# Performance work log

Hardware: AMD Instinct MI355X
Metric: run time of the kernel (lower is better)

## Reference

```python
import jax, jax.numpy as jnp
import numpy as np

B, C_IN, H, W = 4, 512, 188, 188
SHARED_CH = 64
NUM_CLASS = 3
M = 200
NUM_MAX = 500
STRIDE = 8
PCR = (-75.2, -75.2, -2.0, 75.2, 75.2, 4.0)
VOX = (0.1, 0.1, 0.15)
OUT_CH = (2, 1, 3, 2, 1, 3)  # center, center_z, dim, rot, iou, hm
MIN_RADIUS = 2.0
OVERLAP = 0.1
INIT_BIAS = -2.19


def conv3x3(x, w):
    return jax.lax.conv_general_dilated(x, w, (1, 1), 'SAME',
                                        dimension_numbers=('NCHW', 'OIHW', 'NCHW'))


def bn_relu(x, p):
    # p: [4, C] = gamma, beta, running_mean, running_var (inference-mode BN)
    g, b, m, v = p[0], p[1], p[2], p[3]
    scale = (g * jax.lax.rsqrt(v + 1e-5))[None, :, None, None]
    y = (x - m[None, :, None, None]) * scale + b[None, :, None, None]
    return jax.nn.relu(y)


def gaussian_radius(height, width, min_overlap):
    # Faithful to OpenPCDet centernet_utils.gaussian_radius
    b1 = height + width
    c1 = width * height * (1 - min_overlap) / (1 + min_overlap)
    sq1 = jnp.sqrt(jnp.maximum(b1 * b1 - 4.0 * c1, 0.0))
    r1 = (b1 + sq1) / 2.0
    b2 = 2.0 * (height + width)
    c2 = (1 - min_overlap) * width * height
    sq2 = jnp.sqrt(jnp.maximum(b2 * b2 - 16.0 * c2, 0.0))
    r2 = (b2 + sq2) / 2.0
    a3 = 4.0 * min_overlap
    b3 = -2.0 * min_overlap * (height + width)
    c3 = (min_overlap - 1.0) * width * height
    sq3 = jnp.sqrt(jnp.maximum(b3 * b3 - 4.0 * a3 * c3, 0.0))
    r3 = (b3 + sq3) / 2.0
    return jnp.minimum(jnp.minimum(r1, r2), r3)


def assign_targets(gt_boxes):
    # gt_boxes: [B, M, 8] = x, y, z, dx, dy, dz, heading, class(1..NUM_CLASS)
    x, y, z = gt_boxes[..., 0], gt_boxes[..., 1], gt_boxes[..., 2]
    dx, dy, dz = gt_boxes[..., 3], gt_boxes[..., 4], gt_boxes[..., 5]
    heading = gt_boxes[..., 6]
    cls = jax.lax.stop_gradient(gt_boxes[..., 7]).astype(jnp.int32)

    cx = jnp.clip((x - PCR[0]) / VOX[0] / STRIDE, 0.0, W - 0.5)  # [B,M]
    cy = jnp.clip((y - PCR[1]) / VOX[1] / STRIDE, 0.0, H - 0.5)
    cxi = jax.lax.stop_gradient(jnp.floor(cx)).astype(jnp.int32)  # .int() trunc == floor (>=0)
    cyi = jax.lax.stop_gradient(jnp.floor(cy)).astype(jnp.int32)

    dxp = dx / VOX[0] / STRIDE
    dyp = dy / VOX[1] / STRIDE
    r = gaussian_radius(dxp, dyp, OVERLAP)
    r = jnp.maximum(jnp.floor(jax.lax.stop_gradient(r)), MIN_RADIUS)  # clamp_min(r.int(), 2)
    sigma = (2.0 * r + 1.0) / 6.0
    valid = (dx > 0) & (dy > 0)  # [B,M]

    ox = jnp.arange(W, dtype=jnp.int32)[None, None, :] - cxi[..., None]  # [B,M,W]
    oy = jnp.arange(H, dtype=jnp.int32)[None, None, :] - cyi[..., None]  # [B,M,H]
    d2 = (oy.astype(jnp.float32) ** 2)[:, :, :, None] + (ox.astype(jnp.float32) ** 2)[:, :, None, :]
    g = jnp.exp(-d2 / (2.0 * sigma * sigma)[:, :, None, None])  # [B,M,H,W]
    win = (jnp.abs(oy)[:, :, :, None] <= r[:, :, None, None]) & \
          (jnp.abs(ox)[:, :, None, :] <= r[:, :, None, None])
    g = jnp.where(win & valid[:, :, None, None], g, 0.0)

    # per-class max-splat (draw_gaussian_to_heatmap uses torch.max overlap)
    heatmap = jnp.stack(
        [jnp.max(jnp.where((cls == c + 1)[:, :, None, None], g, 0.0), axis=1)
         for c in range(NUM_CLASS)], axis=1)  # [B,NUM_CLASS,H,W]

    vf = valid.astype(gt_boxes.dtype)
    vals = jnp.stack([cx - cxi.astype(cx.dtype), cy - cyi.astype(cy.dtype), z,
                      jnp.log(dx), jnp.log(dy), jnp.log(dz),
                      jnp.cos(heading), jnp.sin(heading)], axis=-1) * vf[..., None]
    target_boxes = jnp.zeros((B, NUM_MAX, 8), gt_boxes.dtype).at[:, :M].set(vals)
    ind_vals = (cyi * W + cxi) * valid.astype(jnp.int32)
    inds = jnp.zeros((B, NUM_MAX), jnp.int32).at[:, :M].set(ind_vals)
    mask = jnp.zeros((B, NUM_MAX), jnp.int32).at[:, :M].set(valid.astype(jnp.int32))
    return heatmap, target_boxes, inds, mask


def setup_inputs() -> dict:
    key = jax.random.key(0)
    ks = jax.random.split(key, 16)
    spatial_features = jax.random.normal(ks[0], (B, C_IN, H, W), jnp.float32)
    x = jax.random.uniform(ks[1], (B, M), minval=-70.0, maxval=70.0)
    y = jax.random.uniform(ks[2], (B, M), minval=-70.0, maxval=70.0)
    z = jax.random.uniform(ks[3], (B, M), minval=-1.0, maxval=1.0)
    dx = jax.random.uniform(ks[4], (B, M), minval=1.5, maxval=5.0)
    dy = jax.random.uniform(ks[5], (B, M), minval=1.5, maxval=5.0)
    dz = jax.random.uniform(ks[6], (B, M), minval=1.0, maxval=3.0)
    hd = jax.random.uniform(ks[7], (B, M), minval=-np.pi, maxval=np.pi)
    cls = jax.random.randint(ks[8], (B, M), 1, NUM_CLASS + 1).astype(jnp.float32)
    gt_boxes = jnp.stack([x, y, z, dx, dy, dz, hd, cls], axis=-1)

    def mk_bn(k, lead):
        kk = jax.random.split(k, 4)
        g = 1.0 + 0.1 * jax.random.normal(kk[0], lead + (SHARED_CH,))
        b = 0.1 * jax.random.normal(kk[1], lead + (SHARED_CH,))
        m = 0.1 * jax.random.normal(kk[2], lead + (SHARED_CH,))
        v = jax.random.uniform(kk[3], lead + (SHARED_CH,), minval=0.5, maxval=1.5)
        return jnp.stack([g, b, m, v], axis=len(lead))

    w_shared = jax.random.normal(ks[9], (SHARED_CH, C_IN, 3, 3)) * (1.0 / np.sqrt(C_IN * 9))
    bn_shared = mk_bn(ks[10], ())
    w1_heads = jax.random.normal(ks[11], (6, SHARED_CH, SHARED_CH, 3, 3)) * (1.0 / np.sqrt(SHARED_CH * 9))
    bn_heads = mk_bn(ks[12], (6,))
    w2_heads = jax.random.normal(ks[13], (6, 3, SHARED_CH, 3, 3)) * (1.0 / np.sqrt(SHARED_CH * 9))
    b2_heads = jnp.zeros((6, 3), jnp.float32).at[5].set(INIT_BIAS)  # hm branch bias = -2.19
    return {'spatial_features': spatial_features, 'gt_boxes': gt_boxes,
            'w_shared': w_shared, 'bn_shared': bn_shared,
            'w1_heads': w1_heads, 'bn_heads': bn_heads,
            'w2_heads': w2_heads, 'b2_heads': b2_heads}


def reference(spatial_features, gt_boxes, w_shared, bn_shared,
              w1_heads, bn_heads, w2_heads, b2_heads):
    shared = bn_relu(conv3x3(spatial_features, w_shared), bn_shared)  # [B,64,H,W]

    def branch(w1, bnp, w2, b2):
        h = bn_relu(conv3x3(shared, w1), bnp)
        return conv3x3(h, w2) + b2[None, :, None, None]  # [B,3,H,W] (out padded to 3)

    outs = jax.vmap(branch)(w1_heads, bn_heads, w2_heads, b2_heads)  # [6,B,3,H,W]
    head_out = jnp.concatenate([outs[i, :, :OUT_CH[i]] for i in range(6)], axis=1)  # [B,12,H,W]

    heatmap, target_boxes, inds, mask = assign_targets(gt_boxes)
    return head_out, heatmap, target_boxes, inds, mask
```

## Files before the change

kernel.cpp:

```cpp
#include <hip/hip_runtime.h>
#include <hip/hip_bf16.h>

#define HWD 188
#define NPX (HWD*HWD)
#define NB 4
#define CIN 512
#define CH 64
#define MBOX 200
#define NMAX 500

#define HEAD_SZ (NB*12*NPX)
#define HM_OFF  HEAD_SZ
#define TB_OFF  (HM_OFF + NB*3*NPX)
#define IND_OFF (TB_OFF + NB*NMAX*8)
#define MSK_OFF (IND_OFF + NB*NMAX)

typedef short sh8 __attribute__((ext_vector_type(8)));
typedef float f4 __attribute__((ext_vector_type(4)));
typedef unsigned short us4 __attribute__((ext_vector_type(4)));

__device__ __constant__ int d_cum[6]  = {0, 2, 3, 6, 8, 9};
__device__ __constant__ int d_outc[6] = {2, 1, 3, 2, 1, 3};

__device__ __forceinline__ unsigned short bf16_bits(float v) {
  union { __hip_bfloat16 h; unsigned short u; } cv;
  cv.h = __float2bfloat16(v);
  return cv.u;
}

__global__ __launch_bounds__(256) void wprep(
    const float* __restrict__ ws_, const float* __restrict__ w1_,
    const float* __restrict__ w2_, unsigned short* __restrict__ w1b,
    unsigned short* __restrict__ w2b, unsigned short* __restrict__ w3b) {
  int e = blockIdx.x * 256 + threadIdx.x;
  const int N1 = 9 * 64 * 512;
  const int N2 = 6 * 9 * 64 * 64;
  const int N3 = 6 * 9 * 16 * 64;
  if (e < N1) {
    int tap = e / (64 * 512); int r = e % (64 * 512);
    int oc = r / 512; int ic = r % 512;
    w1b[e] = bf16_bits(ws_[(oc * 512 + ic) * 9 + tap]);
  } else if (e < N1 + N2) {
    int f = e - N1;
    int h = f / (9 * 64 * 64); int r = f % (9 * 64 * 64);
    int tap = r / (64 * 64); int r2 = r % (64 * 64);
    int oc = r2 / 64; int ic = r2 % 64;
    w2b[f] = bf16_bits(w1_[((h * 64 + oc) * 64 + ic) * 9 + tap]);
  } else if (e < N1 + N2 + N3) {
    int f = e - N1 - N2;
    int h = f / (9 * 16 * 64); int r = f % (9 * 16 * 64);
    int tap = r / (16 * 64); int r2 = r % (16 * 64);
    int oc = r2 / 64; int ic = r2 % 64;
    float v = (oc < 3) ? w2_[((h * 3 + oc) * 64 + ic) * 9 + tap] : 0.f;
    w3b[f] = bf16_bits(v);
  }
}

__global__ __launch_bounds__(256) void conv1_mfma(
    const float* __restrict__ sf,
    const unsigned short* __restrict__ wb,
    const float* __restrict__ bnp,
    unsigned short* __restrict__ outp) {
  __shared__ __align__(16) short s_in[10 * 34 * 32];
  const int t = threadIdx.x;
  const int b = blockIdx.y;
  const int rt = blockIdx.x / 6, ct = blockIdx.x % 6;
  const int y0 = rt * 8, x0 = ct * 32;
  const int w = t >> 6, lane = t & 63, ln = lane & 15, kg = lane >> 4;

  f4 acc[4][4];
#pragma unroll
  for (int i = 0; i < 4; ++i)
#pragma unroll
    for (int j = 0; j < 4; ++j) acc[i][j] = (f4){0.f, 0.f, 0.f, 0.f};

  for (int ic0 = 0; ic0 < CIN; ic0 += 32) {
    __syncthreads();
    for (int idx = t; idx < 2720; idx += 256) {
      int c = idx % 34; int rem = idx / 34;
      int r = rem % 10; int iq = rem / 10;
      int gy = y0 - 1 + r, gx = x0 - 1 + c;
      float v0 = 0.f, v1 = 0.f, v2 = 0.f, v3 = 0.f;
      if (gy >= 0 && gy < HWD && gx >= 0 && gx < HWD) {
        const float* p = sf + ((b * CIN + ic0 + iq * 4) * HWD + gy) * HWD + gx;
        v0 = p[0]; v1 = p[NPX]; v2 = p[2 * NPX]; v3 = p[3 * NPX];
      }
      us4 pk = {bf16_bits(v0), bf16_bits(v1), bf16_bits(v2), bf16_bits(v3)};
      *reinterpret_cast<us4*>(&s_in[(r * 34 + c) * 32 + iq * 4]) = pk;
    }
    __syncthreads();
    for (int tap = 0; tap < 9; ++tap) {
      const int ky = tap / 3, kx = tap % 3;
      sh8 af[4];
#pragma unroll
      for (int ot = 0; ot < 4; ++ot)
        af[ot] = *reinterpret_cast<const sh8*>(
            wb + (tap * 64 + ot * 16 + ln) * CIN + ic0 + kg * 8);
#pragma unroll
      for (int nt = 0; nt < 4; ++nt) {
        const int rr = 2 * w + (nt >> 1) + ky;
        const int cc = (nt & 1) * 16 + ln + kx;
        sh8 bf = *reinterpret_cast<const sh8*>(&s_in[(rr * 34 + cc) * 32 + kg * 8]);
#pragma unroll
        for (int ot = 0; ot < 4; ++ot)
          acc[ot][nt] = __builtin_amdgcn_mfma_f32_16x16x32_bf16(
              af[ot], bf, acc[ot][nt], 0, 0, 0);
      }
    }
  }
#pragma unroll
  for (int ot = 0; ot < 4; ++ot) {
    const int ocb = ot * 16 + kg * 4;
    f4 g4 = *reinterpret_cast<const f4*>(bnp + ocb);
    f4 b4 = *reinterpret_cast<const f4*>(bnp + 64 + ocb);
    f4 m4 = *reinterpret_cast<const f4*>(bnp + 128 + ocb);
    f4 v4 = *reinterpret_cast<const f4*>(bnp + 192 + ocb);
    f4 sc, bi;
#pragma unroll
    for (int j = 0; j < 4; ++j) {
      sc[j] = g4[j] * rsqrtf(v4[j] + 1e-5f);
      bi[j] = b4[j] - m4[j] * sc[j];
    }
#pragma unroll
    for (int nt = 0; nt < 4; ++nt) {
      int y = y0 + 2 * w + (nt >> 1);
      int x = x0 + (nt & 1) * 16 + ln;
      if (y < HWD && x < HWD) {
        us4 pk;
#pragma unroll
        for (int j = 0; j < 4; ++j)
          pk[j] = bf16_bits(fmaxf(acc[ot][nt][j] * sc[j] + bi[j], 0.f));
        *reinterpret_cast<us4*>(outp + ((b * HWD + y) * HWD + x) * 64 + ocb) = pk;
      }
    }
  }
}

template<int OCT, int EPI>
__global__ __launch_bounds__(256) void conv_head_mfma(
    const unsigned short* __restrict__ inp,
    const unsigned short* __restrict__ wb0,
    const float* __restrict__ bn0,
    const float* __restrict__ b2,
    unsigned short* __restrict__ outp0,
    float* __restrict__ hout,
    int h_base, long long stride) {
  __shared__ __align__(16) short s_in[10 * 34 * 32];
  const int t = threadIdx.x;
  const int b = blockIdx.y;
  const int h = h_base + blockIdx.z;
  const int rt = blockIdx.x / 6, ct = blockIdx.x % 6;
  const int y0 = rt * 8, x0 = ct * 32;
  const int w = t >> 6, lane = t & 63, ln = lane & 15, kg = lane >> 4;

  const unsigned short* wb = wb0 + h * (9 * OCT * 16 * 64);
  const unsigned short* in_t = (EPI == 1) ? inp + h * stride : inp;

  f4 acc[OCT][4];
#pragma unroll
  for (int i = 0; i < OCT; ++i)
#pragma unroll
    for (int j = 0; j < 4; ++j) acc[i][j] = (f4){0.f, 0.f, 0.f, 0.f};

  for (int ic0 = 0; ic0 < CH; ic0 += 32) {
    __syncthreads();
    for (int idx = t; idx < 1360; idx += 256) {
      int icg = idx & 3; int pix = idx >> 2;
      int c = pix % 34; int r = pix / 34;
      int gy = y0 - 1 + r, gx = x0 - 1 + c;
      sh8 v = (sh8){0, 0, 0, 0, 0, 0, 0, 0};
      if (gy >= 0 && gy < HWD && gx >= 0 && gx < HWD)
        v = *reinterpret_cast<const sh8*>(
            &in_t[((b * HWD + gy) * HWD + gx) * 64 + ic0 + icg * 8]);
      *reinterpret_cast<sh8*>(&s_in[(r * 34 + c) * 32 + icg * 8]) = v;
    }
    __syncthreads();
    for (int tap = 0; tap < 9; ++tap) {
      const int ky = tap / 3, kx = tap % 3;
      sh8 af[OCT];
#pragma unroll
      for (int ot = 0; ot < OCT; ++ot)
        af[ot] = *reinterpret_cast<const sh8*>(
            wb + (tap * OCT * 16 + ot * 16 + ln) * 64 + ic0 + kg * 8);
#pragma unroll
      for (int nt = 0; nt < 4; ++nt) {
        const int rr = 2 * w + (nt >> 1) + ky;
        const int cc = (nt & 1) * 16 + ln + kx;
        sh8 bf = *reinterpret_cast<const sh8*>(&s_in[(rr * 34 + cc) * 32 + kg * 8]);
#pragma unroll
        for (int ot = 0; ot < OCT; ++ot)
          acc[ot][nt] = __builtin_amdgcn_mfma_f32_16x16x32_bf16(
              af[ot], bf, acc[ot][nt], 0, 0, 0);
      }
    }
  }
  if (EPI == 0) {
    unsigned short* outp = outp0 + h * stride;
#pragma unroll
    for (int ot = 0; ot < OCT; ++ot) {
      const int ocb = ot * 16 + kg * 4;
      const float* bnp = bn0 + h * 256;
      f4 g4 = *reinterpret_cast<const f4*>(bnp + ocb);
      f4 b4 = *reinterpret_cast<const f4*>(bnp + 64 + ocb);
      f4 m4 = *reinterpret_cast<const f4*>(bnp + 128 + ocb);
      f4 v4 = *reinterpret_cast<const f4*>(bnp + 192 + ocb);
      f4 sc, bi;
#pragma unroll
      for (int j = 0; j < 4; ++j) {
        sc[j] = g4[j] * rsqrtf(v4[j] + 1e-5f);
        bi[j] = b4[j] - m4[j] * sc[j];
      }
#pragma unroll
      for (int nt = 0; nt < 4; ++nt) {
        int y = y0 + 2 * w + (nt >> 1);
        int x = x0 + (nt & 1) * 16 + ln;
        if (y < HWD && x < HWD) {
          us4 pk;
#pragma unroll
          for (int j = 0; j < 4; ++j)
            pk[j] = bf16_bits(fmaxf(acc[ot][nt][j] * sc[j] + bi[j], 0.f));
          *reinterpret_cast<us4*>(outp + ((b * HWD + y) * HWD + x) * 64 + ocb) = pk;
        }
      }
    }
  } else {
    const int c_off = d_cum[h], noc = d_outc[h];
    const float* bias = b2 + h * 3;
#pragma unroll
    for (int nt = 0; nt < 4; ++nt) {
      int y = y0 + 2 * w + (nt >> 1);
      int x = x0 + (nt & 1) * 16 + ln;
      if (y < HWD && x < HWD) {
#pragma unroll
        for (int j = 0; j < 4; ++j) {
          int oc = kg * 4 + j;
          if (oc < noc)
            hout[(b * 12 + c_off + oc) * NPX + y * HWD + x] =
                acc[0][nt][j] + bias[oc];
        }
      }
    }
  }
}

__global__ __launch_bounds__(256) void targets_kernel(
    const float* __restrict__ gt, float* __restrict__ out, float* __restrict__ boxp) {
  int idx = blockIdx.x * 256 + threadIdx.x;
  if (idx >= NB * NMAX) return;
  int b = idx / NMAX, j = idx - b * NMAX;
  float vals[8] = {0, 0, 0, 0, 0, 0, 0, 0};
  float indf = 0.f, mkf = 0.f;
  if (j < MBOX) {
    const float* g = gt + (b * MBOX + j) * 8;
    float x = g[0], y = g[1], z = g[2], dx = g[3], dy = g[4], dz = g[5];
    float hd = g[6], cls = g[7];
    float cx = (x - (-75.2f)) / 0.1f / 8.0f;
    cx = fminf(fmaxf(cx, 0.0f), (float)HWD - 0.5f);
    float cy = (y - (-75.2f)) / 0.1f / 8.0f;
    cy = fminf(fmaxf(cy, 0.0f), (float)HWD - 0.5f);
    float cxf = floorf(cx), cyf = floorf(cy);
    int cxi = (int)cxf, cyi = (int)cyf;
    float hh = dx / 0.1f / 8.0f;
    float ww = dy / 0.1f / 8.0f;
    const float ov = 0.1f;
    float b1 = hh + ww;
    float c1 = ww * hh * (1.0f - ov) / (1.0f + ov);
    float sq1 = sqrtf(fmaxf(b1 * b1 - 4.0f * c1, 0.0f));
    float r1 = (b1 + sq1) / 2.0f;
    float b2_ = 2.0f * (hh + ww);
    float c2 = (1.0f - ov) * ww * hh;
    float sq2 = sqrtf(fmaxf(b2_ * b2_ - 16.0f * c2, 0.0f));
    float r2 = (b2_ + sq2) / 2.0f;
    float a3 = 4.0f * ov;
    float b3 = -2.0f * ov * (hh + ww);
    float c3 = (ov - 1.0f) * ww * hh;
    float sq3 = sqrtf(fmaxf(b3 * b3 - 4.0f * a3 * c3, 0.0f));
    float r3 = (b3 + sq3) / 2.0f;
    float r = fminf(fminf(r1, r2), r3);
    r = fmaxf(floorf(r), 2.0f);
    float sigma = (2.0f * r + 1.0f) / 6.0f;
    float inv2s2 = 1.0f / (2.0f * sigma * sigma);
    bool valid = (dx > 0.0f) && (dy > 0.0f);
    float vf = valid ? 1.0f : 0.0f;
    vals[0] = (cx - cxf) * vf;
    vals[1] = (cy - cyf) * vf;
    vals[2] = z * vf;
    vals[3] = logf(dx) * vf;
    vals[4] = logf(dy) * vf;
    vals[5] = logf(dz) * vf;
    vals[6] = cosf(hd) * vf;
    vals[7] = sinf(hd) * vf;
    indf = (float)((cyi * HWD + cxi) * (valid ? 1 : 0));
    mkf = vf;
    float* bp = boxp + (b * MBOX + j) * 8;
    bp[0] = cxf; bp[1] = cyf; bp[2] = r; bp[3] = inv2s2;
    bp[4] = valid ? cls : 0.0f; bp[5] = 0.f; bp[6] = 0.f; bp[7] = 0.f;
  }
  float* tb = out + TB_OFF + (b * NMAX + j) * 8;
#pragma unroll
  for (int k = 0; k < 8; ++k) tb[k] = vals[k];
  out[IND_OFF + b * NMAX + j] = indf;
  out[MSK_OFF + b * NMAX + j] = mkf;
}

__global__ __launch_bounds__(256) void heatmap_kernel(
    const float* __restrict__ boxp, float* __restrict__ out) {
  __shared__ float s_bp[MBOX][5];
  const int t = threadIdx.x, b = blockIdx.y;
  for (int e = t; e < MBOX * 5; e += 256) {
    int j = e / 5, k = e - j * 5;
    s_bp[j][k] = boxp[(b * MBOX + j) * 8 + k];
  }
  __syncthreads();
  int p = blockIdx.x * 256 + t;
  if (p >= NPX) return;
  int y = p / HWD, x = p - y * HWD;
  float a0 = 0.f, a1 = 0.f, a2 = 0.f;
  for (int j = 0; j < MBOX; ++j) {
    int c = (int)s_bp[j][4];
    if (c == 0) continue;
    float ox = (float)x - s_bp[j][0];
    float oy = (float)y - s_bp[j][1];
    float r = s_bp[j][2];
    if (fabsf(ox) <= r && fabsf(oy) <= r) {
      float gg = expf(-(ox * ox + oy * oy) * s_bp[j][3]);
      if (c == 1) a0 = fmaxf(a0, gg);
      else if (c == 2) a1 = fmaxf(a1, gg);
      else a2 = fmaxf(a2, gg);
    }
  }
  int base = HM_OFF + (b * 3 * HWD + y) * HWD + x;
  out[base] = a0;
  out[base + NPX] = a1;
  out[base + 2 * NPX] = a2;
}

extern "C" void kernel_launch(void* const* d_in, const int* in_sizes, int n_in,
                              void* d_out, int out_size, void* d_ws, size_t ws_size,
                              hipStream_t stream) {
  (void)in_sizes; (void)n_in; (void)out_size;
  const float* sf = (const float*)d_in[0];
  const float* gt = (const float*)d_in[1];
  const float* w_shared = (const float*)d_in[2];
  const float* bn_shared = (const float*)d_in[3];
  const float* w1 = (const float*)d_in[4];
  const float* bnH = (const float*)d_in[5];
  const float* w2 = (const float*)d_in[6];
  const float* b2 = (const float*)d_in[7];
  float* out = (float*)d_out;
  char* ws = (char*)d_ws;

  const size_t SH = (size_t)NB * NPX * 64 * 2;
  unsigned short* shared_t = (unsigned short*)ws;
  unsigned short* w1b = (unsigned short*)(ws + SH);
  unsigned short* w2b = (unsigned short*)(ws + SH + 589824);
  unsigned short* w3b = (unsigned short*)(ws + SH + 589824 + 442368);
  float* boxp = (float*)(ws + SH + 589824 + 442368 + 110592);
  unsigned short* tmp0 = (unsigned short*)(ws + SH + 589824 + 442368 + 110592 + 25600);

  const size_t need_wide = SH + 589824 + 442368 + 110592 + 25600 + 6 * SH;
  const bool wide = ws_size >= need_wide;
  const long long tstride = wide ? (long long)(SH / 2) : 0LL;

  wprep<<<2232, 256, 0, stream>>>(w_shared, w1, w2, w1b, w2b, w3b);
  conv1_mfma<<<dim3(144, NB), 256, 0, stream>>>(sf, w1b, bn_shared, shared_t);

  if (wide) {
    conv_head_mfma<4, 0><<<dim3(144, NB, 6), 256, 0, stream>>>(
        shared_t, w2b, bnH, nullptr, tmp0, nullptr, 0, tstride);
    conv_head_mfma<1, 1><<<dim3(144, NB, 6), 256, 0, stream>>>(
        tmp0, w3b, nullptr, b2, nullptr, out, 0, tstride);
  } else {
    for (int h = 0; h < 6; ++h) {
      conv_head_mfma<4, 0><<<dim3(144, NB), 256, 0, stream>>>(
          shared_t, w2b, bnH, nullptr, tmp0, nullptr, h, 0);
      conv_head_mfma<1, 1><<<dim3(144, NB), 256, 0, stream>>>(
          tmp0, w3b, nullptr, b2, nullptr, out, h, 0);
    }
  }

  targets_kernel<<<(NB * NMAX + 255) / 256, 256, 0, stream>>>(gt, out, boxp);
  heatmap_kernel<<<dim3((NPX + 255) / 256, NB), 256, 0, stream>>>(boxp, out);
}
```

Measured before the change: 664.6 us.

## Split-K conv1 over input channels with atomic fp32 accumulation and padded LDS

```diff
diff --git a/kernel.cpp b/kernel.cpp
--- a/kernel.cpp
+++ b/kernel.cpp
@@ -15,6 +15,8 @@
 #define IND_OFF (TB_OFF + NB*NMAX*8)
 #define MSK_OFF (IND_OFF + NB*NMAX)
 
+#define PXS 40
+
 typedef short sh8 __attribute__((ext_vector_type(8)));
 typedef float f4 __attribute__((ext_vector_type(4)));
 typedef unsigned short us4 __attribute__((ext_vector_type(4)));
@@ -33,13 +35,14 @@
     const float* __restrict__ w2_, unsigned short* __restrict__ w1b,
     unsigned short* __restrict__ w2b, unsigned short* __restrict__ w3b) {
   int e = blockIdx.x * 256 + threadIdx.x;
-  const int N1 = 9 * 64 * 512;
+  const int N1 = 9 * 16 * 64 * 32;
   const int N2 = 6 * 9 * 64 * 64;
   const int N3 = 6 * 9 * 16 * 64;
   if (e < N1) {
-    int tap = e / (64 * 512); int r = e % (64 * 512);
-    int oc = r / 512; int ic = r % 512;
-    w1b[e] = bf16_bits(ws_[(oc * 512 + ic) * 9 + tap]);
+    int icr = e & 31; int r1 = e >> 5;
+    int oc = r1 & 63; int r2 = r1 >> 6;
+    int icq = r2 & 15; int tap = r2 >> 4;
+    w1b[e] = bf16_bits(ws_[(oc * 512 + icq * 32 + icr) * 9 + tap]);
   } else if (e < N1 + N2) {
     int f = e - N1;
     int h = f / (9 * 64 * 64); int r = f % (9 * 64 * 64);
@@ -56,14 +59,22 @@
   }
 }
 
+__global__ __launch_bounds__(256) void zeroacc(f4* __restrict__ p, int n4) {
+  int i = blockIdx.x * 256 + threadIdx.x;
+  if (i < n4) p[i] = (f4){0.f, 0.f, 0.f, 0.f};
+}
+
+template<int SPLIT>
 __global__ __launch_bounds__(256) void conv1_mfma(
     const float* __restrict__ sf,
     const unsigned short* __restrict__ wb,
     const float* __restrict__ bnp,
+    float* __restrict__ accf,
     unsigned short* __restrict__ outp) {
-  __shared__ __align__(16) short s_in[10 * 34 * 32];
+  __shared__ __align__(16) short s_in[10 * 34 * PXS];
   const int t = threadIdx.x;
   const int b = blockIdx.y;
+  const int ks = SPLIT ? blockIdx.z : 0;
   const int rt = blockIdx.x / 6, ct = blockIdx.x % 6;
   const int y0 = rt * 8, x0 = ct * 32;
   const int w = t >> 6, lane = t & 63, ln = lane & 15, kg = lane >> 4;
@@ -74,7 +85,10 @@
 #pragma unroll
     for (int j = 0; j < 4; ++j) acc[i][j] = (f4){0.f, 0.f, 0.f, 0.f};
 
-  for (int ic0 = 0; ic0 < CIN; ic0 += 32) {
+  const int NSTEP = SPLIT ? 4 : 16;
+  for (int s = 0; s < NSTEP; ++s) {
+    const int icq = ks * 4 + s;
+    const int ic0 = icq * 32;
     __syncthreads();
     for (int idx = t; idx < 2720; idx += 256) {
       int c = idx % 34; int rem = idx / 34;
@@ -86,7 +100,7 @@
         v0 = p[0]; v1 = p[NPX]; v2 = p[2 * NPX]; v3 = p[3 * NPX];
       }
       us4 pk = {bf16_bits(v0), bf16_bits(v1), bf16_bits(v2), bf16_bits(v3)};
-      *reinterpret_cast<us4*>(&s_in[(r * 34 + c) * 32 + iq * 4]) = pk;
+      *reinterpret_cast<us4*>(&s_in[(r * 34 + c) * PXS + iq * 4]) = pk;
     }
     __syncthreads();
     for (int tap = 0; tap < 9; ++tap) {
@@ -95,12 +109,12 @@
 #pragma unroll
       for (int ot = 0; ot < 4; ++ot)
         af[ot] = *reinterpret_cast<const sh8*>(
-            wb + (tap * 64 + ot * 16 + ln) * CIN + ic0 + kg * 8);
+            wb + (((tap * 16 + icq) * 64) + ot * 16 + ln) * 32 + kg * 8);
 #pragma unroll
       for (int nt = 0; nt < 4; ++nt) {
         const int rr = 2 * w + (nt >> 1) + ky;
         const int cc = (nt & 1) * 16 + ln + kx;
-        sh8 bf = *reinterpret_cast<const sh8*>(&s_in[(rr * 34 + cc) * 32 + kg * 8]);
+        sh8 bf = *reinterpret_cast<const sh8*>(&s_in[(rr * 34 + cc) * PXS + kg * 8]);
 #pragma unroll
         for (int ot = 0; ot < 4; ++ot)
           acc[ot][nt] = __builtin_amdgcn_mfma_f32_16x16x32_bf16(
@@ -108,31 +122,75 @@
       }
     }
   }
-#pragma unroll
-  for (int ot = 0; ot < 4; ++ot) {
-    const int ocb = ot * 16 + kg * 4;
-    f4 g4 = *reinterpret_cast<const f4*>(bnp + ocb);
-    f4 b4 = *reinterpret_cast<const f4*>(bnp + 64 + ocb);
-    f4 m4 = *reinterpret_cast<const f4*>(bnp + 128 + ocb);
-    f4 v4 = *reinterpret_cast<const f4*>(bnp + 192 + ocb);
-    f4 sc, bi;
-#pragma unroll
-    for (int j = 0; j < 4; ++j) {
-      sc[j] = g4[j] * rsqrtf(v4[j] + 1e-5f);
-      bi[j] = b4[j] - m4[j] * sc[j];
-    }
-#pragma unroll
-    for (int nt = 0; nt < 4; ++nt) {
-      int y = y0 + 2 * w + (nt >> 1);
-      int x = x0 + (nt & 1) * 16 + ln;
-      if (y < HWD && x < HWD) {
-        us4 pk;
-#pragma unroll
-        for (int j = 0; j < 4; ++j)
-          pk[j] = bf16_bits(fmaxf(acc[ot][nt][j] * sc[j] + bi[j], 0.f));
-        *reinterpret_cast<us4*>(outp + ((b * HWD + y) * HWD + x) * 64 + ocb) = pk;
-      }
-    }
+  if (SPLIT) {
+#pragma unroll
+    for (int ot = 0; ot < 4; ++ot) {
+#pragma unroll
+      for (int nt = 0; nt < 4; ++nt) {
+        int y = y0 + 2 * w + (nt >> 1);
+        int x = x0 + (nt & 1) * 16 + ln;
+        if (y < HWD && x < HWD) {
+          float* p = accf + ((b * HWD + y) * HWD + x) * 64 + ot * 16 + kg * 4;
+#pragma unroll
+          for (int j = 0; j < 4; ++j) atomicAdd(p + j, acc[ot][nt][j]);
+        }
+      }
+    }
+  } else {
+#pragma unroll
+    for (int ot = 0; ot < 4; ++ot) {
+      const int ocb = ot * 16 + kg * 4;
+      f4 g4 = *reinterpret_cast<const f4*>(bnp + ocb);
+      f4 b4 = *reinterpret_cast<const f4*>(bnp + 64 + ocb);
+      f4 m4 = *reinterpret_cast<const f4*>(bnp + 128 + ocb);
+      f4 v4 = *reinterpret_cast<const f4*>(bnp + 192 + ocb);
+      f4 sc, bi;
+#pragma unroll
+      for (int j = 0; j < 4; ++j) {
+        sc[j] = g4[j] * rsqrtf(v4[j] + 1e-5f);
+        bi[j] = b4[j] - m4[j] * sc[j];
+      }
+#pragma unroll
+      for (int nt = 0; nt < 4; ++nt) {
+        int y = y0 + 2 * w + (nt >> 1);
+        int x = x0 + (nt & 1) * 16 + ln;
+        if (y < HWD && x < HWD) {
+          us4 pk;
+#pragma unroll
+          for (int j = 0; j < 4; ++j)
+            pk[j] = bf16_bits(fmaxf(acc[ot][nt][j] * sc[j] + bi[j], 0.f));
+          *reinterpret_cast<us4*>(outp + ((b * HWD + y) * HWD + x) * 64 + ocb) = pk;
+        }
+      }
+    }
+  }
+}
+
+__global__ __launch_bounds__(256) void bn_pack(
+    const float* __restrict__ accf, const float* __restrict__ bnp,
+    unsigned short* __restrict__ outp) {
+  __shared__ float s_sc[64], s_bi[64];
+  const int t = threadIdx.x;
+  if (t < 64) {
+    float g = bnp[t], be = bnp[64 + t], m = bnp[128 + t], v = bnp[192 + t];
+    float sc = g * rsqrtf(v + 1e-5f);
+    s_sc[t] = sc; s_bi[t] = be - m * sc;
+  }
+  __syncthreads();
+  int idx = blockIdx.x * 256 + t;
+  if (idx >= NB * NPX * 4) return;
+  int px = idx >> 2, q = idx & 3;
+  const float* p = accf + (long long)px * 64 + q * 16;
+  unsigned short* o = outp + (long long)px * 64 + q * 16;
+  const int ocb = q * 16;
+#pragma unroll
+  for (int k = 0; k < 4; ++k) {
+    f4 v4 = *reinterpret_cast<const f4*>(p + k * 4);
+    us4 pk;
+#pragma unroll
+    for (int j = 0; j < 4; ++j)
+      pk[j] = bf16_bits(fmaxf(v4[j] * s_sc[ocb + k * 4 + j] + s_bi[ocb + k * 4 + j], 0.f));
+    *reinterpret_cast<us4*>(o + k * 4) = pk;
   }
 }
 
@@ -145,7 +203,7 @@
     unsigned short* __restrict__ outp0,
     float* __restrict__ hout,
     int h_base, long long stride) {
-  __shared__ __align__(16) short s_in[10 * 34 * 32];
+  __shared__ __align__(16) short s_in[10 * 34 * PXS];
   const int t = threadIdx.x;
   const int b = blockIdx.y;
   const int h = h_base + blockIdx.z;
@@ -172,7 +230,7 @@
       if (gy >= 0 && gy < HWD && gx >= 0 && gx < HWD)
         v = *reinterpret_cast<const sh8*>(
             &in_t[((b * HWD + gy) * HWD + gx) * 64 + ic0 + icg * 8]);
-      *reinterpret_cast<sh8*>(&s_in[(r * 34 + c) * 32 + icg * 8]) = v;
+      *reinterpret_cast<sh8*>(&s_in[(r * 34 + c) * PXS + icg * 8]) = v;
     }
     __syncthreads();
     for (int tap = 0; tap < 9; ++tap) {
@@ -186,7 +244,7 @@
       for (int nt = 0; nt < 4; ++nt) {
         const int rr = 2 * w + (nt >> 1) + ky;
         const int cc = (nt & 1) * 16 + ln + kx;
-        sh8 bf = *reinterpret_cast<const sh8*>(&s_in[(rr * 34 + cc) * 32 + kg * 8]);
+        sh8 bf = *reinterpret_cast<const sh8*>(&s_in[(rr * 34 + cc) * PXS + kg * 8]);
 #pragma unroll
         for (int ot = 0; ot < OCT; ++ot)
           acc[ot][nt] = __builtin_amdgcn_mfma_f32_16x16x32_bf16(
@@ -356,14 +414,28 @@
   unsigned short* w2b = (unsigned short*)(ws + SH + 589824);
   unsigned short* w3b = (unsigned short*)(ws + SH + 589824 + 442368);
   float* boxp = (float*)(ws + SH + 589824 + 442368 + 110592);
-  unsigned short* tmp0 = (unsigned short*)(ws + SH + 589824 + 442368 + 110592 + 25600);
-
-  const size_t need_wide = SH + 589824 + 442368 + 110592 + 25600 + 6 * SH;
-  const bool wide = ws_size >= need_wide;
+  const size_t off_acc = SH + 589824 + 442368 + 110592 + 25600;
+  float* accf = (float*)(ws + off_acc);
+  unsigned short* tmp0 = (unsigned short*)(ws + off_acc);
+
+  const size_t ACC_B = (size_t)NB * NPX * 64 * 4;
+  const bool split = ws_size >= off_acc + ACC_B;
+  const bool wide = ws_size >= off_acc + 6 * SH;
   const long long tstride = wide ? (long long)(SH / 2) : 0LL;
 
   wprep<<<2232, 256, 0, stream>>>(w_shared, w1, w2, w1b, w2b, w3b);
-  conv1_mfma<<<dim3(144, NB), 256, 0, stream>>>(sf, w1b, bn_shared, shared_t);
+
+  if (split) {
+    const int n4 = NB * NPX * 16;
+    zeroacc<<<(n4 + 255) / 256, 256, 0, stream>>>((f4*)accf, n4);
+    conv1_mfma<1><<<dim3(144, NB, 4), 256, 0, stream>>>(
+        sf, w1b, nullptr, accf, nullptr);
+    bn_pack<<<(NB * NPX * 4 + 255) / 256, 256, 0, stream>>>(
+        accf, bn_shared, shared_t);
+  } else {
+    conv1_mfma<0><<<dim3(144, NB), 256, 0, stream>>>(
+        sf, w1b, bn_shared, nullptr, shared_t);
+  }
 
   if (wide) {
     conv_head_mfma<4, 0><<<dim3(144, NB, 6), 256, 0, stream>>>(
```

After: 834.8 us. 25.6% more time.

## Double-buffer conv1 input staging with vectorized loads, 512 threads, padded LDS

Applied to the files above, without the earlier changes.

```diff
diff --git a/kernel.cpp b/kernel.cpp
--- a/kernel.cpp
+++ b/kernel.cpp
@@ -15,6 +15,8 @@
 #define IND_OFF (TB_OFF + NB*NMAX*8)
 #define MSK_OFF (IND_OFF + NB*NMAX)
 
+#define PXS 40
+
 typedef short sh8 __attribute__((ext_vector_type(8)));
 typedef float f4 __attribute__((ext_vector_type(4)));
 typedef unsigned short us4 __attribute__((ext_vector_type(4)));
@@ -33,13 +35,14 @@
     const float* __restrict__ w2_, unsigned short* __restrict__ w1b,
     unsigned short* __restrict__ w2b, unsigned short* __restrict__ w3b) {
   int e = blockIdx.x * 256 + threadIdx.x;
-  const int N1 = 9 * 64 * 512;
+  const int N1 = 9 * 16 * 64 * 32;
   const int N2 = 6 * 9 * 64 * 64;
   const int N3 = 6 * 9 * 16 * 64;
   if (e < N1) {
-    int tap = e / (64 * 512); int r = e % (64 * 512);
-    int oc = r / 512; int ic = r % 512;
-    w1b[e] = bf16_bits(ws_[(oc * 512 + ic) * 9 + tap]);
+    int icr = e & 31; int r1 = e >> 5;
+    int oc = r1 & 63; int r2 = r1 >> 6;
+    int icq = r2 & 15; int tap = r2 >> 4;
+    w1b[e] = bf16_bits(ws_[(oc * 512 + icq * 32 + icr) * 9 + tap]);
   } else if (e < N1 + N2) {
     int f = e - N1;
     int h = f / (9 * 64 * 64); int r = f % (9 * 64 * 64);
@@ -56,61 +59,112 @@
   }
 }
 
-__global__ __launch_bounds__(256) void conv1_mfma(
+__device__ __forceinline__ void stage_load(
+    const float* __restrict__ sf, int b, int ic0, int y0, int x0, int item,
+    f4 v[4]) {
+#pragma unroll
+  for (int j = 0; j < 4; ++j) v[j] = (f4){0.f, 0.f, 0.f, 0.f};
+  int icg = item & 7; int pc = item >> 3;
+  int cc = pc % 10; int r = pc / 10;
+  int gy = y0 - 1 + r;
+  int gx0 = x0 - 4 + cc * 4;
+  if (gy >= 0 && gy < HWD) {
+    const float* p = sf + (((long long)b * CIN + ic0 + icg * 4) * HWD + gy) * HWD + gx0;
+    if (gx0 >= 0 && gx0 + 3 < HWD) {
+#pragma unroll
+      for (int j = 0; j < 4; ++j) v[j] = *reinterpret_cast<const f4*>(p + j * NPX);
+    } else {
+#pragma unroll
+      for (int k = 0; k < 4; ++k) {
+        int gx = gx0 + k;
+        if (gx >= 0 && gx < HWD) {
+#pragma unroll
+          for (int j = 0; j < 4; ++j) v[j][k] = p[j * NPX + k];
+        }
+      }
+    }
+  }
+}
+
+__device__ __forceinline__ void stage_write(short* buf, int item, const f4 v[4]) {
+  int icg = item & 7; int pc = item >> 3;
+  int cc = pc % 10; int r = pc / 10;
+#pragma unroll
+  for (int k = 0; k < 4; ++k) {
+    int col = cc * 4 + k - 3;
+    if (col >= 0 && col < 34) {
+      us4 pk = {bf16_bits(v[0][k]), bf16_bits(v[1][k]),
+                bf16_bits(v[2][k]), bf16_bits(v[3][k])};
+      *reinterpret_cast<us4*>(&buf[(r * 34 + col) * PXS + icg * 4]) = pk;
+    }
+  }
+}
+
+__global__ __launch_bounds__(512, 4) void conv1_mfma(
     const float* __restrict__ sf,
     const unsigned short* __restrict__ wb,
     const float* __restrict__ bnp,
     unsigned short* __restrict__ outp) {
-  __shared__ __align__(16) short s_in[10 * 34 * 32];
+  __shared__ __align__(16) short s_in[2][10 * 34 * PXS];
   const int t = threadIdx.x;
   const int b = blockIdx.y;
   const int rt = blockIdx.x / 6, ct = blockIdx.x % 6;
   const int y0 = rt * 8, x0 = ct * 32;
   const int w = t >> 6, lane = t & 63, ln = lane & 15, kg = lane >> 4;
-
-  f4 acc[4][4];
-#pragma unroll
-  for (int i = 0; i < 4; ++i)
+  const int rp = w & 3, oh = w >> 2;
+
+  f4 acc[2][4];
+#pragma unroll
+  for (int i = 0; i < 2; ++i)
 #pragma unroll
     for (int j = 0; j < 4; ++j) acc[i][j] = (f4){0.f, 0.f, 0.f, 0.f};
 
-  for (int ic0 = 0; ic0 < CIN; ic0 += 32) {
-    __syncthreads();
-    for (int idx = t; idx < 2720; idx += 256) {
-      int c = idx % 34; int rem = idx / 34;
-      int r = rem % 10; int iq = rem / 10;
-      int gy = y0 - 1 + r, gx = x0 - 1 + c;
-      float v0 = 0.f, v1 = 0.f, v2 = 0.f, v3 = 0.f;
-      if (gy >= 0 && gy < HWD && gx >= 0 && gx < HWD) {
-        const float* p = sf + ((b * CIN + ic0 + iq * 4) * HWD + gy) * HWD + gx;
-        v0 = p[0]; v1 = p[NPX]; v2 = p[2 * NPX]; v3 = p[3 * NPX];
-      }
-      us4 pk = {bf16_bits(v0), bf16_bits(v1), bf16_bits(v2), bf16_bits(v3)};
-      *reinterpret_cast<us4*>(&s_in[(r * 34 + c) * 32 + iq * 4]) = pk;
-    }
-    __syncthreads();
+  const bool has2 = (t < 800 - 512);
+  f4 st0[4], st1[4];
+
+  stage_load(sf, b, 0, y0, x0, t, st0);
+  if (has2) stage_load(sf, b, 0, y0, x0, t + 512, st1);
+  stage_write(s_in[0], t, st0);
+  if (has2) stage_write(s_in[0], t + 512, st1);
+  __syncthreads();
+
+  for (int s = 0; s < 16; ++s) {
+    const short* cur = s_in[s & 1];
+    if (s < 15) {
+      stage_load(sf, b, (s + 1) * 32, y0, x0, t, st0);
+      if (has2) stage_load(sf, b, (s + 1) * 32, y0, x0, t + 512, st1);
+    }
+    const int icq = s;
+#pragma unroll
     for (int tap = 0; tap < 9; ++tap) {
       const int ky = tap / 3, kx = tap % 3;
-      sh8 af[4];
-#pragma unroll
-      for (int ot = 0; ot < 4; ++ot)
-        af[ot] = *reinterpret_cast<const sh8*>(
-            wb + (tap * 64 + ot * 16 + ln) * CIN + ic0 + kg * 8);
+      sh8 af[2];
+#pragma unroll
+      for (int i = 0; i < 2; ++i)
+        af[i] = *reinterpret_cast<const sh8*>(
+            wb + (((tap * 16 + icq) * 64) + (2 * oh + i) * 16 + ln) * 32 + kg * 8);
 #pragma unroll
       for (int nt = 0; nt < 4; ++nt) {
-        const int rr = 2 * w + (nt >> 1) + ky;
+        const int rr = 2 * rp + (nt >> 1) + ky;
         const int cc = (nt & 1) * 16 + ln + kx;
-        sh8 bf = *reinterpret_cast<const sh8*>(&s_in[(rr * 34 + cc) * 32 + kg * 8]);
-#pragma unroll
-        for (int ot = 0; ot < 4; ++ot)
-          acc[ot][nt] = __builtin_amdgcn_mfma_f32_16x16x32_bf16(
-              af[ot], bf, acc[ot][nt], 0, 0, 0);
-      }
-    }
-  }
-#pragma unroll
-  for (int ot = 0; ot < 4; ++ot) {
-    const int ocb = ot * 16 + kg * 4;
+        sh8 bf = *reinterpret_cast<const sh8*>(&cur[(rr * 34 + cc) * PXS + kg * 8]);
+#pragma unroll
+        for (int i = 0; i < 2; ++i)
+          acc[i][nt] = __builtin_amdgcn_mfma_f32_16x16x32_bf16(
+              af[i], bf, acc[i][nt], 0, 0, 0);
+      }
+    }
+    if (s < 15) {
+      short* nxt = s_in[(s & 1) ^ 1];
+      stage_write(nxt, t, st0);
+      if (has2) stage_write(nxt, t + 512, st1);
+    }
+    __syncthreads();
+  }
+
+#pragma unroll
+  for (int i = 0; i < 2; ++i) {
+    const int ocb = (2 * oh + i) * 16 + kg * 4;
     f4 g4 = *reinterpret_cast<const f4*>(bnp + ocb);
     f4 b4 = *reinterpret_cast<const f4*>(bnp + 64 + ocb);
     f4 m4 = *reinterpret_cast<const f4*>(bnp + 128 + ocb);
@@ -123,13 +177,13 @@
     }
 #pragma unroll
     for (int nt = 0; nt < 4; ++nt) {
-      int y = y0 + 2 * w + (nt >> 1);
+      int y = y0 + 2 * rp + (nt >> 1);
       int x = x0 + (nt & 1) * 16 + ln;
       if (y < HWD && x < HWD) {
         us4 pk;
 #pragma unroll
         for (int j = 0; j < 4; ++j)
-          pk[j] = bf16_bits(fmaxf(acc[ot][nt][j] * sc[j] + bi[j], 0.f));
+          pk[j] = bf16_bits(fmaxf(acc[i][nt][j] * sc[j] + bi[j], 0.f));
         *reinterpret_cast<us4*>(outp + ((b * HWD + y) * HWD + x) * 64 + ocb) = pk;
       }
     }
@@ -145,7 +199,7 @@
     unsigned short* __restrict__ outp0,
     float* __restrict__ hout,
     int h_base, long long stride) {
-  __shared__ __align__(16) short s_in[10 * 34 * 32];
+  __shared__ __align__(16) short s_in[10 * 34 * PXS];
   const int t = threadIdx.x;
   const int b = blockIdx.y;
   const int h = h_base + blockIdx.z;
@@ -172,7 +226,7 @@
       if (gy >= 0 && gy < HWD && gx >= 0 && gx < HWD)
         v = *reinterpret_cast<const sh8*>(
             &in_t[((b * HWD + gy) * HWD + gx) * 64 + ic0 + icg * 8]);
-      *reinterpret_cast<sh8*>(&s_in[(r * 34 + c) * 32 + icg * 8]) = v;
+      *reinterpret_cast<sh8*>(&s_in[(r * 34 + c) * PXS + icg * 8]) = v;
     }
     __syncthreads();
     for (int tap = 0; tap < 9; ++tap) {
@@ -186,7 +240,7 @@
       for (int nt = 0; nt < 4; ++nt) {
         const int rr = 2 * w + (nt >> 1) + ky;
         const int cc = (nt & 1) * 16 + ln + kx;
-        sh8 bf = *reinterpret_cast<const sh8*>(&s_in[(rr * 34 + cc) * 32 + kg * 8]);
+        sh8 bf = *reinterpret_cast<const sh8*>(&s_in[(rr * 34 + cc) * PXS + kg * 8]);
 #pragma unroll
         for (int ot = 0; ot < OCT; ++ot)
           acc[ot][nt] = __builtin_amdgcn_mfma_f32_16x16x32_bf16(
@@ -356,14 +410,15 @@
   unsigned short* w2b = (unsigned short*)(ws + SH + 589824);
   unsigned short* w3b = (unsigned short*)(ws + SH + 589824 + 442368);
   float* boxp = (float*)(ws + SH + 589824 + 442368 + 110592);
-  unsigned short* tmp0 = (unsigned short*)(ws + SH + 589824 + 442368 + 110592 + 25600);
-
-  const size_t need_wide = SH + 589824 + 442368 + 110592 + 25600 + 6 * SH;
-  const bool wide = ws_size >= need_wide;
+  const size_t off_tmp = SH + 589824 + 442368 + 110592 + 25600;
+  unsigned short* tmp0 = (unsigned short*)(ws + off_tmp);
+
+  const bool wide = ws_size >= off_tmp + 6 * SH;
   const long long tstride = wide ? (long long)(SH / 2) : 0LL;
 
   wprep<<<2232, 256, 0, stream>>>(w_shared, w1, w2, w1b, w2b, w3b);
-  conv1_mfma<<<dim3(144, NB), 256, 0, stream>>>(sf, w1b, bn_shared, shared_t);
+
+  conv1_mfma<<<dim3(144, NB), 512, 0, stream>>>(sf, w1b, bn_shared, shared_t);
 
   if (wide) {
     conv_head_mfma<4, 0><<<dim3(144, NB, 6), 256, 0, stream>>>(
```

New measurement: 553.6 us. 16.7% less time.
